# Performance work log

Measured on AMD Instinct MI355X. Metric: run time of the kernel, lower is better.

The kernel has to match this reference:

```python
import math
import jax, jax.numpy as jnp
import numpy as np

NUM_HEADS = 16


def setup_inputs() -> dict:
    key = jax.random.key(0)
    ks = jax.random.split(key, 5)
    B, S, H = 2, 2048, 1024
    hidden_states = jax.random.normal(ks[0], (B, S, H), dtype=jnp.float32)
    # causal lower-triangular float mask [1, 1, S, S], as the module expects
    ltor_mask = jnp.tril(jnp.ones((S, S), dtype=jnp.float32))[None, None, :, :]
    # weights stored pre-transposed: y = x @ W + b (equivalent to torch Linear)
    W_qkv = jax.random.normal(ks[1], (H, 3 * H), dtype=jnp.float32) * (1.0 / math.sqrt(H))
    b_qkv = jnp.zeros((3 * H,), dtype=jnp.float32)
    W_dense = jax.random.normal(ks[2], (H, H), dtype=jnp.float32) * (1.0 / math.sqrt(H))
    b_dense = jnp.zeros((H,), dtype=jnp.float32)
    return {
        "hidden_states": hidden_states,
        "ltor_mask": ltor_mask,
        "W_qkv": W_qkv,
        "b_qkv": b_qkv,
        "W_dense": W_dense,
        "b_dense": b_dense,
    }


def reference(hidden_states, ltor_mask, W_qkv, b_qkv, W_dense, b_dense):
    B, S, H = hidden_states.shape
    nh = NUM_HEADS
    hd = H // nh

    # fused QKV projection: [B, S, 3H] -> split -> [B, nh, S, hd]
    qkv = hidden_states @ W_qkv + b_qkv
    q, k, v = jnp.split(qkv, 3, axis=-1)

    def to_heads(x):
        return x.reshape(B, S, nh, hd).transpose(0, 2, 1, 3)

    q, k, v = to_heads(q), to_heads(k), to_heads(v)

    # scaled dot-product scores [B, nh, S, S]
    scores = jnp.einsum("bhqd,bhkd->bhqk", q, k) / math.sqrt(hd)
    # mul/sub causal masking, exactly as the torch module does
    scores = scores * ltor_mask - 10000.0 * (1.0 - ltor_mask)
    probs = jax.nn.softmax(scores, axis=-1)
    # attention dropout omitted (eval mode / p=0.0)

    ctx = jnp.einsum("bhqk,bhkd->bhqd", probs, v)
    ctx = ctx.transpose(0, 2, 1, 3).reshape(B, S, H)

    out = ctx @ W_dense + b_dense
    # output dropout omitted (eval mode / p=0.0)
    return out
```

## Files before the change

### kernel.cpp

```cpp
#include <hip/hip_runtime.h>
#include <math.h>

#define BATCH 2
#define SEQ   2048
#define HID   1024
#define NHEAD 16
#define HDIM  64
#define MTOT  (BATCH * SEQ)
#define QKVN  (3 * HID)
#define HBUF  ((size_t)BATCH * NHEAD * SEQ * HDIM)

typedef _Float16 f16x8 __attribute__((ext_vector_type(8)));
typedef _Float16 f16x4 __attribute__((ext_vector_type(4)));
typedef float    f32x4 __attribute__((ext_vector_type(4)));

#define MFMA16(a, b, c) __builtin_amdgcn_mfma_f32_16x16x32_f16((a), (b), (c), 0, 0, 0)

#define GLDS16(gp, lp) __builtin_amdgcn_global_load_lds( \
    (const __attribute__((address_space(1))) void*)(gp), \
    (__attribute__((address_space(3))) void*)(lp), 16, 0, 0)

#if __has_builtin(__builtin_amdgcn_exp2f)
#define EXP2F(x) __builtin_amdgcn_exp2f(x)
#else
#define EXP2F(x) exp2f(x)
#endif

#define SCALE2 0.18033688011f
#define MASK2  -14426.950408f
#define BIAS2  -4.0f

__global__ __launch_bounds__(256) void prep_kernel(
    const float* __restrict__ hs, const float* __restrict__ Wqkv,
    const float* __restrict__ Wd, _Float16* __restrict__ A_h,
    _Float16* __restrict__ outQ, _Float16* __restrict__ outD)
{
    __shared__ _Float16 T[32][36];
    const int gid = blockIdx.x;
    const int tid = threadIdx.x;
    if (gid < 2048) {
        const int ci = gid * 256 + tid;
        const int m = ci >> 7, cc = ci & 127;
        const int g = cc >> 2, c = cc & 3;
        const float* src = hs + (size_t)m * 1024 + cc * 8;
        f16x8 o;
#pragma unroll
        for (int j = 0; j < 8; ++j) o[j] = (_Float16)src[j];
        *(f16x8*)(A_h + (size_t)m * 1024 + g * 32 + ((c ^ (m & 3)) << 3)) = o;
        return;
    }
    const int tb = gid - 2048;
    const int bx = tb & 127, k0 = (tb >> 7) * 32;
    const float* in;
    _Float16* out;
    int N, n0;
    if (bx < 96) { in = Wqkv; out = outQ; N = QKVN; n0 = bx * 32; }
    else         { in = Wd;   out = outD; N = HID;  n0 = (bx - 96) * 32; }
    {
        const int r = tid >> 3, c4 = (tid & 7) * 4;
        float4 v = *(const float4*)(in + (size_t)(k0 + r) * N + n0 + c4);
        T[r][c4 + 0] = (_Float16)v.x;
        T[r][c4 + 1] = (_Float16)v.y;
        T[r][c4 + 2] = (_Float16)v.z;
        T[r][c4 + 3] = (_Float16)v.w;
    }
    __syncthreads();
    {
        const int nn = tid >> 3, k4 = (tid & 7) * 4;
        const int n = n0 + nn;
        f16x4 o;
        o[0] = T[k4 + 0][nn]; o[1] = T[k4 + 1][nn];
        o[2] = T[k4 + 2][nn]; o[3] = T[k4 + 3][nn];
        const int pos = ((k4 >> 3) ^ (n & 3)), half = (k4 >> 2) & 1;
        *(f16x4*)(out + (size_t)n * 1024 + k0 + pos * 8 + half * 4) = o;
    }
}

template<int EPI, int TM>
__global__ __launch_bounds__(256) void mfma_gemm(
    const _Float16* __restrict__ A, const _Float16* __restrict__ Bt,
    const float* __restrict__ bias, void* __restrict__ Cout,
    int M, int N, int K)
{
    __shared__ _Float16 As[TM * 32];
    __shared__ _Float16 Bs[128 * 32];
    constexpr int TI = TM / 32;
    constexpr int AR = TM / 4;

    const int tid = threadIdx.x;
    const int w = tid >> 6, l = tid & 63;
    const int a = l & 15, q4 = l >> 4;
    const int m0 = blockIdx.y * TM, n0 = blockIdx.x * 128;
    const int wm = (w >> 1) * (TM / 2), wn = (w & 1) * 64;

    f32x4 acc[TI][4];
#pragma unroll
    for (int i = 0; i < TI; ++i)
#pragma unroll
        for (int j = 0; j < 4; ++j) acc[i][j] = (f32x4){0.f, 0.f, 0.f, 0.f};

    const _Float16* gA = A + (size_t)(m0 + w * AR + (l >> 2)) * K + (l & 3) * 8;
    const _Float16* gB = Bt + (size_t)(n0 + w * 32 + (l >> 2)) * K + (l & 3) * 8;
    _Float16* sA = As + w * AR * 32;
    _Float16* sB = Bs + w * 1024;

    for (int k0 = 0; k0 < K; k0 += 32) {
#pragma unroll
        for (int u = 0; u < TM / 64; ++u)
            GLDS16(gA + (size_t)u * 16 * K + k0, sA + u * 512);
        GLDS16(gB + k0,          sB);
        GLDS16(gB + 16 * K + k0, sB + 512);
        __syncthreads();

        f16x8 af[TI], bf[4];
        const int pa = (q4 ^ (a & 3)) << 3;
#pragma unroll
        for (int i = 0; i < TI; ++i)
            af[i] = *(const f16x8*)&As[(wm + 16 * i + a) * 32 + pa];
#pragma unroll
        for (int j = 0; j < 4; ++j)
            bf[j] = *(const f16x8*)&Bs[(wn + 16 * j + a) * 32 + pa];
#pragma unroll
        for (int i = 0; i < TI; ++i)
#pragma unroll
            for (int j = 0; j < 4; ++j)
                acc[i][j] = MFMA16(af[i], bf[j], acc[i][j]);
        __syncthreads();
    }

    if (EPI == 0) {
        _Float16* base = (_Float16*)Cout;
#pragma unroll
        for (int j = 0; j < 4; ++j) {
            const int n = n0 + wn + 16 * j + a;
            const float bv = bias[n];
            const int t = n >> 10, h = (n >> 6) & 15, d = n & 63;
#pragma unroll
            for (int i = 0; i < TI; ++i) {
                const int mb = m0 + wm + 16 * i + q4 * 4;
                const int bb = mb >> 11, sb = mb & 2047;
                if (t == 2) {
                    f16x4 ov;
#pragma unroll
                    for (int r = 0; r < 4; ++r)
                        ov[r] = (_Float16)(acc[i][j][r] + bv);
                    const size_t off =
                        ((size_t)((bb * 16 + h) * 64 + d)) * 2048
                        + (sb & ~63)
                        + ((((sb >> 3) & 7) ^ (d & 7)) << 3) + (sb & 7);
                    *(f16x4*)(base + 3 * HBUF + off) = ov;
                } else if (t == 1) {
#pragma unroll
                    for (int r = 0; r < 4; ++r) {
                        const int s = sb + r;
                        const _Float16 val = (_Float16)(acc[i][j][r] + bv);
                        const int dk = ((((d >> 3) ^ (s & 7)) & 7) << 3) | (d & 7);
                        base[HBUF + ((size_t)(bb * 16 + h) * 2048 + s) * 64 + dk] = val;
                    }
                } else {
#pragma unroll
                    for (int r = 0; r < 4; ++r) {
                        const _Float16 val = (_Float16)(acc[i][j][r] + bv);
                        base[((size_t)(bb * 16 + h) * 2048 + sb + r) * 64 + d] = val;
                    }
                }
            }
        }
    } else {
        float* C = (float*)Cout;
#pragma unroll
        for (int j = 0; j < 4; ++j) {
            const int n = n0 + wn + 16 * j + a;
            const float bv = bias[n];
#pragma unroll
            for (int i = 0; i < TI; ++i)
#pragma unroll
                for (int r = 0; r < 4; ++r) {
                    const int m = m0 + wm + 16 * i + q4 * 4 + r;
                    C[(size_t)m * N + n] = acc[i][j][r] + bv;
                }
        }
    }
}

__global__ __launch_bounds__(256, 2) void attn_mfma(
    const _Float16* __restrict__ qb, const _Float16* __restrict__ kb,
    const _Float16* __restrict__ vtb, _Float16* __restrict__ ctx)
{
    __shared__ _Float16 Ks[2][64 * 64];
    __shared__ _Float16 VT[2][64 * 64];
    __shared__ _Float16 Ps[4][16 * 64];

    const int bid = blockIdx.x;
    const int jj = bid >> 3;
    const int bhIdx = (bid & 7) * 4 + (jj >> 4);
    const int p = jj & 15;
    const int b = bhIdx >> 4, h = bhIdx & 15;
    const int tid = threadIdx.x;
    const int w = tid >> 6, l = tid & 63;
    const int a = l & 15, q4 = l >> 4, a7 = a & 7;
    const size_t bh  = ((size_t)b * NHEAD + h) * SEQ;
    const size_t bhd = ((size_t)b * NHEAD + h) * 64;

    const int qHi = (31 - p) * 64 + w * 16;
    const int qLo = p * 64 + w * 16;
    const int ntiles = 32 - p;

    f16x8 qfh[2], qfl[2];
    {
        const _Float16* qp = qb + (bh + qHi + a) * 64;
        qfh[0] = *(const f16x8*)(qp + q4 * 8);
        qfh[1] = *(const f16x8*)(qp + 32 + q4 * 8);
        const _Float16* ql = qb + (bh + qLo + a) * 64;
        qfl[0] = *(const f16x8*)(ql + q4 * 8);
        qfl[1] = *(const f16x8*)(ql + 32 + q4 * 8);
    }

    f32x4 Oh[4], Ol[4];
#pragma unroll
    for (int c = 0; c < 4; ++c) {
        Oh[c] = (f32x4){0.f, 0.f, 0.f, 0.f};
        Ol[c] = (f32x4){0.f, 0.f, 0.f, 0.f};
    }
    float lh = 0.f, ll = 0.f;

    const _Float16* kg = kb + (bh + w * 16) * 64 + l * 8;
    const int vrow = w * 16 + (l >> 3);
    const _Float16* vg = vtb + (bhd + vrow) * 2048 + (l & 7) * 8;
    _Float16* pbuf = &Ps[w][0];
    const int p0 = (q4 ^ a7) << 3;

    auto stage = [&](int t, int buf) {
        _Float16* ksl = &Ks[buf][0] + w * 1024 + l * 8;
        const _Float16* kt = kg + (size_t)t * 4096;
        GLDS16(kt,       ksl);
        GLDS16(kt + 512, ksl + 512);
        _Float16* vtl = &VT[buf][0] + vrow * 64 + (l & 7) * 8;
        GLDS16(vg + t * 64,            vtl);
        GLDS16(vg + t * 64 + 8 * 2048, vtl + 512);
    };

    stage(0, 0);

    for (int t = 0; t < ntiles; ++t) {
        __syncthreads();
        if (t + 1 < ntiles) stage(t + 1, (t + 1) & 1);

        const _Float16* ksb  = &Ks[t & 1][0];
        const _Float16* vbuf = &VT[t & 1][0];
        const int kt0 = t * 64;
        const bool doLo = (t <= p);

        f32x4 sh[4], sl[4];
#pragma unroll
        for (int n0 = 0; n0 < 4; ++n0) {
            f16x8 kf0 = *(const f16x8*)&ksb[(n0 * 16 + a) * 64 + p0];
            f16x8 kf1 = *(const f16x8*)&ksb[(n0 * 16 + a) * 64 + (p0 ^ 32)];
            f32x4 c = (f32x4){0.f, 0.f, 0.f, 0.f};
            c = MFMA16(kf0, qfh[0], c);
            c = MFMA16(kf1, qfh[1], c);
            sh[n0] = c;
            if (doLo) {
                f32x4 d = (f32x4){0.f, 0.f, 0.f, 0.f};
                d = MFMA16(kf0, qfl[0], d);
                d = MFMA16(kf1, qfl[1], d);
                sl[n0] = d;
            }
        }

        auto half_step = [&](f32x4 st[4], float& lrun, f32x4* O,
                             const bool maskT, const int qbase) {
            if (maskT) {
#pragma unroll
                for (int n0 = 0; n0 < 4; ++n0)
#pragma unroll
                    for (int r = 0; r < 4; ++r) {
                        const int kgl = kt0 + n0 * 16 + q4 * 4 + r;
                        st[n0][r] = (kgl > qbase + a) ? MASK2
                                                      : fmaf(st[n0][r], SCALE2, BIAS2);
                    }
            } else {
#pragma unroll
                for (int n0 = 0; n0 < 4; ++n0)
#pragma unroll
                    for (int r = 0; r < 4; ++r)
                        st[n0][r] = fmaf(st[n0][r], SCALE2, BIAS2);
            }
            float ls = 0.f;
#pragma unroll
            for (int n0 = 0; n0 < 4; ++n0)
#pragma unroll
                for (int r = 0; r < 4; ++r) {
                    const float pe = EXP2F(st[n0][r]);
                    st[n0][r] = pe;
                    ls += pe;
                }
            lrun += ls;
#pragma unroll
            for (int n0 = 0; n0 < 4; ++n0) {
                f16x4 pk;
#pragma unroll
                for (int r = 0; r < 4; ++r) pk[r] = (_Float16)st[n0][r];
                const int pos = (2 * n0 + (q4 >> 1)) ^ a7;
                *(f16x4*)&pbuf[a * 64 + pos * 8 + ((q4 & 1) << 2)] = pk;
            }
            f16x8 pf0 = *(const f16x8*)&pbuf[a * 64 + p0];
            f16x8 pf1 = *(const f16x8*)&pbuf[a * 64 + (p0 ^ 32)];
#pragma unroll
            for (int c = 0; c < 4; ++c) {
                f16x8 vf0 = *(const f16x8*)&vbuf[(c * 16 + a) * 64 + p0];
                f16x8 vf1 = *(const f16x8*)&vbuf[(c * 16 + a) * 64 + (p0 ^ 32)];
                O[c] = MFMA16(vf0, pf0, O[c]);
                O[c] = MFMA16(vf1, pf1, O[c]);
            }
        };

        half_step(sh, lh, Oh, t == 31 - p, qHi);
        if (doLo) half_step(sl, ll, Ol, t == p, qLo);
    }

    auto finish = [&](float lrun, const f32x4* O, const int qbase) {
        float lt = lrun;
        lt += __shfl_xor(lt, 16);
        lt += __shfl_xor(lt, 32);
        const float inv = 1.0f / lt;
        const size_t row = (size_t)b * SEQ + qbase + a;
#pragma unroll
        for (int c = 0; c < 4; ++c) {
            const int d0 = c * 16 + q4 * 4;
            const int kcol = h * 64 + (d0 & ~31)
                           + ((((d0 >> 3) & 3) ^ (a & 3)) << 3) + (d0 & 7);
            f16x4 ov;
#pragma unroll
            for (int r = 0; r < 4; ++r) ov[r] = (_Float16)(O[c][r] * inv);
            *(f16x4*)(ctx + row * HID + kcol) = ov;
        }
    };
    finish(lh, Oh, qHi);
    finish(ll, Ol, qLo);
}

extern "C" void kernel_launch(void* const* d_in, const int* in_sizes, int n_in,
                              void* d_out, int out_size, void* d_ws, size_t ws_size,
                              hipStream_t stream) {
    const float* hs   = (const float*)d_in[0];
    const float* Wqkv = (const float*)d_in[2];
    const float* bqkv = (const float*)d_in[3];
    const float* Wd   = (const float*)d_in[4];
    const float* bd   = (const float*)d_in[5];

    _Float16* A_h   = (_Float16*)d_ws;
    _Float16* WqkvT = A_h + (size_t)MTOT * HID;
    _Float16* WdT   = WqkvT + (size_t)QKVN * HID;
    _Float16* qbuf  = WdT + (size_t)HID * HID;
    _Float16* ctxb  = qbuf + 4 * HBUF;

    prep_kernel<<<6144, 256, 0, stream>>>(hs, Wqkv, Wd, A_h, WqkvT, WdT);

    mfma_gemm<0, 128><<<dim3(QKVN / 128, MTOT / 128), 256, 0, stream>>>(
        A_h, WqkvT, bqkv, (void*)qbuf, MTOT, QKVN, HID);

    attn_mfma<<<512, 256, 0, stream>>>(
        qbuf, qbuf + HBUF, qbuf + 3 * HBUF, ctxb);

    mfma_gemm<1, 64><<<dim3(HID / 128, MTOT / 64), 256, 0, stream>>>(
        ctxb, WdT, bd, d_out, MTOT, HID, HID);
}
```

Before: 194.4 us.

## Replace QKV GEMM with 256x256-tile 8-wave pipelined kernel using K=64 stages

Result: no change. 190.6 us (-2.0%).

```diff
diff --git a/kernel.cpp b/kernel.cpp
--- a/kernel.cpp
+++ b/kernel.cpp
@@ -41,12 +41,12 @@
     if (gid < 2048) {
         const int ci = gid * 256 + tid;
         const int m = ci >> 7, cc = ci & 127;
-        const int g = cc >> 2, c = cc & 3;
         const float* src = hs + (size_t)m * 1024 + cc * 8;
         f16x8 o;
 #pragma unroll
         for (int j = 0; j < 8; ++j) o[j] = (_Float16)src[j];
-        *(f16x8*)(A_h + (size_t)m * 1024 + g * 32 + ((c ^ (m & 3)) << 3)) = o;
+        *(f16x8*)(A_h + (size_t)m * 1024 + ((cc >> 3) << 6)
+                  + (((cc & 7) ^ (m & 7)) << 3)) = o;
         return;
     }
     const int tb = gid - 2048;
@@ -54,8 +54,9 @@
     const float* in;
     _Float16* out;
     int N, n0;
-    if (bx < 96) { in = Wqkv; out = outQ; N = QKVN; n0 = bx * 32; }
-    else         { in = Wd;   out = outD; N = HID;  n0 = (bx - 96) * 32; }
+    bool isQ;
+    if (bx < 96) { in = Wqkv; out = outQ; N = QKVN; n0 = bx * 32; isQ = true; }
+    else         { in = Wd;   out = outD; N = HID;  n0 = (bx - 96) * 32; isQ = false; }
     {
         const int r = tid >> 3, c4 = (tid & 7) * 4;
         float4 v = *(const float4*)(in + (size_t)(k0 + r) * N + n0 + c4);
@@ -71,8 +72,180 @@
         f16x4 o;
         o[0] = T[k4 + 0][nn]; o[1] = T[k4 + 1][nn];
         o[2] = T[k4 + 2][nn]; o[3] = T[k4 + 3][nn];
-        const int pos = ((k4 >> 3) ^ (n & 3)), half = (k4 >> 2) & 1;
-        *(f16x4*)(out + (size_t)n * 1024 + k0 + pos * 8 + half * 4) = o;
+        if (isQ) {
+            const int cin = (((k0 >> 5) & 1) << 2) | (k4 >> 3);
+            const int pos = cin ^ (n & 7);
+            *(f16x4*)(out + (size_t)n * 1024 + (k0 & ~63) + pos * 8 + (k4 & 7)) = o;
+        } else {
+            const int pos = ((k4 >> 3) ^ (n & 3)), half = (k4 >> 2) & 1;
+            *(f16x4*)(out + (size_t)n * 1024 + k0 + pos * 8 + half * 4) = o;
+        }
+    }
+}
+
+__global__ __launch_bounds__(512, 2) void qkv_gemm8(
+    const _Float16* __restrict__ A, const _Float16* __restrict__ Bt,
+    const float* __restrict__ bias, _Float16* __restrict__ base)
+{
+    __shared__ _Float16 S[2][2][16384];
+    const int tid = threadIdx.x;
+    const int w = tid >> 6, l = tid & 63;
+    const int a = l & 15, q4 = l >> 4, a7 = a & 7;
+    const int xc = blockIdx.x & 7, loc = blockIdx.x >> 3;
+    const int bx = (xc & 1) * 6 + loc % 6;
+    const int by = (xc >> 1) * 4 + loc / 6;
+    const int m0 = by * 256, n0 = bx * 256;
+    const int wm = (w >> 2) * 128, wn = (w & 3) * 64;
+
+    const int srow = tid >> 3;
+    const int scol = (tid & 7) * 8;
+    const _Float16* gAs = A  + (size_t)(m0 + srow) * 1024 + scol;
+    const _Float16* gBs = Bt + (size_t)(n0 + srow) * 1024 + scol;
+
+    auto stage_u = [&](int u, int kt, int sl) {
+        const size_t ko = (size_t)kt * 64;
+        if (u < 4)
+            GLDS16(gAs + (size_t)u * 65536 + ko, &S[sl][0][0] + u * 4096 + tid * 8);
+        else
+            GLDS16(gBs + (size_t)(u - 4) * 65536 + ko, &S[sl][1][0] + (u - 4) * 4096 + tid * 8);
+    };
+
+#pragma unroll
+    for (int u = 0; u < 8; ++u) stage_u(u, 0, 0);
+#pragma unroll
+    for (int u = 0; u < 8; ++u) stage_u(u, 1, 1);
+    asm volatile("s_waitcnt vmcnt(8)" ::: "memory");
+    __builtin_amdgcn_sched_barrier(0);
+    __builtin_amdgcn_s_barrier();
+
+    f32x4 acc[8][4];
+#pragma unroll
+    for (int i = 0; i < 8; ++i)
+#pragma unroll
+        for (int j = 0; j < 4; ++j) acc[i][j] = (f32x4){0.f, 0.f, 0.f, 0.f};
+
+#define FRG(SP, row_, ks_) \
+    (*(const f16x8*)&(SP)[(row_) * 64 + ((((ks_) * 4 + q4) ^ a7) << 3)])
+
+    for (int t = 0; t < 16; ++t) {
+        const int sl = t & 1, nsl = sl ^ 1;
+        const _Float16* sA = &S[sl][0][0];
+        const _Float16* sB = &S[sl][1][0];
+        const bool st = (t >= 1) & (t < 15);
+
+        f16x8 afL[4][2], afH[4][2], bfL[2][2], bfH[2][2];
+
+#pragma unroll
+        for (int i = 0; i < 4; ++i) {
+            afL[i][0] = FRG(sA, wm + i * 16 + a, 0);
+            afL[i][1] = FRG(sA, wm + i * 16 + a, 1);
+        }
+#pragma unroll
+        for (int j = 0; j < 2; ++j) {
+            bfL[j][0] = FRG(sB, wn + j * 16 + a, 0);
+            bfL[j][1] = FRG(sB, wn + j * 16 + a, 1);
+        }
+        if (st) { stage_u(0, t + 1, nsl); stage_u(1, t + 1, nsl); stage_u(2, t + 1, nsl); }
+        __builtin_amdgcn_s_barrier();
+        asm volatile("s_waitcnt lgkmcnt(0)" ::: "memory");
+        __builtin_amdgcn_s_setprio(1);
+#pragma unroll
+        for (int i = 0; i < 4; ++i)
+#pragma unroll
+            for (int j = 0; j < 2; ++j) {
+                acc[i][j] = MFMA16(afL[i][0], bfL[j][0], acc[i][j]);
+                acc[i][j] = MFMA16(afL[i][1], bfL[j][1], acc[i][j]);
+            }
+        __builtin_amdgcn_s_setprio(0);
+        __builtin_amdgcn_s_barrier();
+
+#pragma unroll
+        for (int j = 0; j < 2; ++j) {
+            bfH[j][0] = FRG(sB, wn + 32 + j * 16 + a, 0);
+            bfH[j][1] = FRG(sB, wn + 32 + j * 16 + a, 1);
+        }
+        if (st) { stage_u(3, t + 1, nsl); stage_u(4, t + 1, nsl); stage_u(5, t + 1, nsl); }
+        __builtin_amdgcn_s_barrier();
+        asm volatile("s_waitcnt lgkmcnt(0)" ::: "memory");
+        __builtin_amdgcn_s_setprio(1);
+#pragma unroll
+        for (int i = 0; i < 4; ++i)
+#pragma unroll
+            for (int j = 0; j < 2; ++j) {
+                acc[i][j + 2] = MFMA16(afL[i][0], bfH[j][0], acc[i][j + 2]);
+                acc[i][j + 2] = MFMA16(afL[i][1], bfH[j][1], acc[i][j + 2]);
+            }
+        __builtin_amdgcn_s_setprio(0);
+        __builtin_amdgcn_s_barrier();
+
+#pragma unroll
+        for (int i = 0; i < 4; ++i) {
+            afH[i][0] = FRG(sA, wm + 64 + i * 16 + a, 0);
+            afH[i][1] = FRG(sA, wm + 64 + i * 16 + a, 1);
+        }
+        if (st) { stage_u(6, t + 1, nsl); stage_u(7, t + 1, nsl); }
+        __builtin_amdgcn_s_barrier();
+        asm volatile("s_waitcnt lgkmcnt(0)" ::: "memory");
+        __builtin_amdgcn_s_setprio(1);
+#pragma unroll
+        for (int i = 0; i < 4; ++i)
+#pragma unroll
+            for (int j = 0; j < 2; ++j) {
+                acc[i + 4][j + 2] = MFMA16(afH[i][0], bfH[j][0], acc[i + 4][j + 2]);
+                acc[i + 4][j + 2] = MFMA16(afH[i][1], bfH[j][1], acc[i + 4][j + 2]);
+            }
+        __builtin_amdgcn_s_setprio(0);
+        __builtin_amdgcn_s_barrier();
+
+        __builtin_amdgcn_s_setprio(1);
+#pragma unroll
+        for (int i = 0; i < 4; ++i)
+#pragma unroll
+            for (int j = 0; j < 2; ++j) {
+                acc[i + 4][j] = MFMA16(afH[i][0], bfL[j][0], acc[i + 4][j]);
+                acc[i + 4][j] = MFMA16(afH[i][1], bfL[j][1], acc[i + 4][j]);
+            }
+        __builtin_amdgcn_s_setprio(0);
+        asm volatile("s_waitcnt vmcnt(0)" ::: "memory");
+        __builtin_amdgcn_sched_barrier(0);
+        __builtin_amdgcn_s_barrier();
+    }
+#undef FRG
+
+#pragma unroll
+    for (int j = 0; j < 4; ++j) {
+        const int n = n0 + wn + 16 * j + a;
+        const float bv = bias[n];
+        const int tq = n >> 10, h = (n >> 6) & 15, d = n & 63;
+#pragma unroll
+        for (int i = 0; i < 8; ++i) {
+            const int mb = m0 + wm + 16 * i + q4 * 4;
+            const int bb = mb >> 11, sb = mb & 2047;
+            if (tq == 2) {
+                f16x4 ov;
+#pragma unroll
+                for (int r = 0; r < 4; ++r) ov[r] = (_Float16)(acc[i][j][r] + bv);
+                const size_t off =
+                    ((size_t)((bb * 16 + h) * 64 + d)) * 2048
+                    + (sb & ~63)
+                    + ((((sb >> 3) & 7) ^ (d & 7)) << 3) + (sb & 7);
+                *(f16x4*)(base + 3 * HBUF + off) = ov;
+            } else if (tq == 1) {
+#pragma unroll
+                for (int r = 0; r < 4; ++r) {
+                    const int s = sb + r;
+                    const _Float16 val = (_Float16)(acc[i][j][r] + bv);
+                    const int dk = ((((d >> 3) ^ (s & 7)) & 7) << 3) | (d & 7);
+                    base[HBUF + ((size_t)(bb * 16 + h) * 2048 + s) * 64 + dk] = val;
+                }
+            } else {
+#pragma unroll
+                for (int r = 0; r < 4; ++r) {
+                    const _Float16 val = (_Float16)(acc[i][j][r] + bv);
+                    base[((size_t)(bb * 16 + h) * 2048 + sb + r) * 64 + d] = val;
+                }
+            }
+        }
     }
 }
 
@@ -128,45 +301,7 @@
         __syncthreads();
     }
 
-    if (EPI == 0) {
-        _Float16* base = (_Float16*)Cout;
-#pragma unroll
-        for (int j = 0; j < 4; ++j) {
-            const int n = n0 + wn + 16 * j + a;
-            const float bv = bias[n];
-            const int t = n >> 10, h = (n >> 6) & 15, d = n & 63;
-#pragma unroll
-            for (int i = 0; i < TI; ++i) {
-                const int mb = m0 + wm + 16 * i + q4 * 4;
-                const int bb = mb >> 11, sb = mb & 2047;
-                if (t == 2) {
-                    f16x4 ov;
-#pragma unroll
-                    for (int r = 0; r < 4; ++r)
-                        ov[r] = (_Float16)(acc[i][j][r] + bv);
-                    const size_t off =
-                        ((size_t)((bb * 16 + h) * 64 + d)) * 2048
-                        + (sb & ~63)
-                        + ((((sb >> 3) & 7) ^ (d & 7)) << 3) + (sb & 7);
-                    *(f16x4*)(base + 3 * HBUF + off) = ov;
-                } else if (t == 1) {
-#pragma unroll
-                    for (int r = 0; r < 4; ++r) {
-                        const int s = sb + r;
-                        const _Float16 val = (_Float16)(acc[i][j][r] + bv);
-                        const int dk = ((((d >> 3) ^ (s & 7)) & 7) << 3) | (d & 7);
-                        base[HBUF + ((size_t)(bb * 16 + h) * 2048 + s) * 64 + dk] = val;
-                    }
-                } else {
-#pragma unroll
-                    for (int r = 0; r < 4; ++r) {
-                        const _Float16 val = (_Float16)(acc[i][j][r] + bv);
-                        base[((size_t)(bb * 16 + h) * 2048 + sb + r) * 64 + d] = val;
-                    }
-                }
-            }
-        }
-    } else {
+    {
         float* C = (float*)Cout;
 #pragma unroll
         for (int j = 0; j < 4; ++j) {
@@ -357,8 +492,7 @@
 
     prep_kernel<<<6144, 256, 0, stream>>>(hs, Wqkv, Wd, A_h, WqkvT, WdT);
 
-    mfma_gemm<0, 128><<<dim3(QKVN / 128, MTOT / 128), 256, 0, stream>>>(
-        A_h, WqkvT, bqkv, (void*)qbuf, MTOT, QKVN, HID);
+    qkv_gemm8<<<192, 512, 0, stream>>>(A_h, WqkvT, bqkv, qbuf);
 
     attn_mfma<<<512, 256, 0, stream>>>(
         qbuf, qbuf + HBUF, qbuf + 3 * HBUF, ctxb);
```

## Replace QKV GEMM with 256x256-tile, 4-stage pipelined 512-thread MFMA kernel

Applied to the files above, without the earlier changes.

After: 189.1 us. -2.7%, faster.

```diff
diff --git a/kernel.cpp b/kernel.cpp
--- a/kernel.cpp
+++ b/kernel.cpp
@@ -41,12 +41,11 @@
     if (gid < 2048) {
         const int ci = gid * 256 + tid;
         const int m = ci >> 7, cc = ci & 127;
-        const int g = cc >> 2, c = cc & 3;
         const float* src = hs + (size_t)m * 1024 + cc * 8;
         f16x8 o;
 #pragma unroll
         for (int j = 0; j < 8; ++j) o[j] = (_Float16)src[j];
-        *(f16x8*)(A_h + (size_t)m * 1024 + g * 32 + ((c ^ (m & 3)) << 3)) = o;
+        *(f16x8*)(A_h + (size_t)m * 1024 + cc * 8) = o;
         return;
     }
     const int tb = gid - 2048;
@@ -54,8 +53,9 @@
     const float* in;
     _Float16* out;
     int N, n0;
-    if (bx < 96) { in = Wqkv; out = outQ; N = QKVN; n0 = bx * 32; }
-    else         { in = Wd;   out = outD; N = HID;  n0 = (bx - 96) * 32; }
+    bool isQ;
+    if (bx < 96) { in = Wqkv; out = outQ; N = QKVN; n0 = bx * 32; isQ = true; }
+    else         { in = Wd;   out = outD; N = HID;  n0 = (bx - 96) * 32; isQ = false; }
     {
         const int r = tid >> 3, c4 = (tid & 7) * 4;
         float4 v = *(const float4*)(in + (size_t)(k0 + r) * N + n0 + c4);
@@ -71,8 +71,157 @@
         f16x4 o;
         o[0] = T[k4 + 0][nn]; o[1] = T[k4 + 1][nn];
         o[2] = T[k4 + 2][nn]; o[3] = T[k4 + 3][nn];
-        const int pos = ((k4 >> 3) ^ (n & 3)), half = (k4 >> 2) & 1;
-        *(f16x4*)(out + (size_t)n * 1024 + k0 + pos * 8 + half * 4) = o;
+        if (isQ) {
+            *(f16x4*)(out + (size_t)n * 1024 + k0 + k4) = o;
+        } else {
+            const int pos = ((k4 >> 3) ^ (n & 3)), half = (k4 >> 2) & 1;
+            *(f16x4*)(out + (size_t)n * 1024 + k0 + pos * 8 + half * 4) = o;
+        }
+    }
+}
+
+__global__ __launch_bounds__(512, 2) void qkv_gemm8(
+    const _Float16* __restrict__ A, const _Float16* __restrict__ Bt,
+    const float* __restrict__ bias, _Float16* __restrict__ base)
+{
+    __shared__ _Float16 S[4][2][8192];
+    const int tid = threadIdx.x;
+    const int w = tid >> 6, l = tid & 63;
+    const int a = l & 15, q4 = l >> 4;
+    const int xc = blockIdx.x & 7, loc = blockIdx.x >> 3;
+    const int bx = (xc & 1) * 6 + loc % 6;
+    const int by = (xc >> 1) * 4 + loc / 6;
+    const int m0 = by * 256, n0 = bx * 256;
+    const int wm = (w >> 2) * 128, wn = (w & 3) * 64;
+
+    const int csw = (((tid & 3) ^ ((tid >> 3) & 3)) << 3);
+    const _Float16* gAs = A  + (size_t)(m0 + (tid >> 2)) * 1024 + csw;
+    const _Float16* gBs = Bt + (size_t)(n0 + (tid >> 2)) * 1024 + csw;
+
+    auto stage_tile = [&](int kt) {
+        const int s = kt & 3;
+        const size_t ko = (size_t)kt * 32;
+        GLDS16(gAs + ko,          &S[s][0][0] + tid * 8);
+        GLDS16(gAs + 131072 + ko, &S[s][0][0] + 4096 + tid * 8);
+        GLDS16(gBs + ko,          &S[s][1][0] + tid * 8);
+        GLDS16(gBs + 131072 + ko, &S[s][1][0] + 4096 + tid * 8);
+    };
+
+    stage_tile(0); stage_tile(1); stage_tile(2);
+    asm volatile("s_waitcnt vmcnt(8)" ::: "memory");
+    __builtin_amdgcn_sched_barrier(0);
+    __builtin_amdgcn_s_barrier();
+    __builtin_amdgcn_sched_barrier(0);
+
+    f32x4 acc[8][4];
+#pragma unroll
+    for (int i = 0; i < 8; ++i)
+#pragma unroll
+        for (int j = 0; j < 4; ++j) acc[i][j] = (f32x4){0.f, 0.f, 0.f, 0.f};
+
+    const int pc = ((q4 ^ ((a >> 1) & 3)) << 3);
+#define FRG(SP, row_) (*(const f16x8*)&(SP)[(row_) * 32 + pc])
+
+    f16x8 af[8], bf[4];
+    {
+        const _Float16* sA = &S[0][0][0];
+        const _Float16* sB = &S[0][1][0];
+#pragma unroll
+        for (int i = 0; i < 4; ++i) af[i] = FRG(sA, wm + i * 16 + a);
+        bf[0] = FRG(sB, wn + a);
+        bf[1] = FRG(sB, wn + 16 + a);
+    }
+
+#pragma unroll 4
+    for (int t = 0; t < 32; ++t) {
+        const _Float16* sA = &S[t & 3][0][0];
+        const _Float16* sB = &S[t & 3][1][0];
+        if (t <= 28) stage_tile(t + 3);
+
+        __builtin_amdgcn_s_setprio(1);
+#pragma unroll
+        for (int i = 0; i < 4; ++i)
+#pragma unroll
+            for (int j = 0; j < 2; ++j)
+                acc[i][j] = MFMA16(af[i], bf[j], acc[i][j]);
+        __builtin_amdgcn_s_setprio(0);
+
+        bf[2] = FRG(sB, wn + 32 + a);
+        bf[3] = FRG(sB, wn + 48 + a);
+        __builtin_amdgcn_s_setprio(1);
+#pragma unroll
+        for (int i = 0; i < 4; ++i)
+#pragma unroll
+            for (int j = 0; j < 2; ++j)
+                acc[i][j + 2] = MFMA16(af[i], bf[j + 2], acc[i][j + 2]);
+        __builtin_amdgcn_s_setprio(0);
+
+#pragma unroll
+        for (int i = 0; i < 4; ++i) af[i + 4] = FRG(sA, wm + 64 + i * 16 + a);
+        __builtin_amdgcn_s_setprio(1);
+#pragma unroll
+        for (int i = 0; i < 4; ++i)
+#pragma unroll
+            for (int j = 0; j < 2; ++j)
+                acc[i + 4][j + 2] = MFMA16(af[i + 4], bf[j + 2], acc[i + 4][j + 2]);
+#pragma unroll
+        for (int i = 0; i < 4; ++i)
+#pragma unroll
+            for (int j = 0; j < 2; ++j)
+                acc[i + 4][j] = MFMA16(af[i + 4], bf[j], acc[i + 4][j]);
+        __builtin_amdgcn_s_setprio(0);
+
+        if (t < 31) {
+            if (t <= 28)      asm volatile("s_waitcnt vmcnt(8)" ::: "memory");
+            else if (t == 29) asm volatile("s_waitcnt vmcnt(4)" ::: "memory");
+            else              asm volatile("s_waitcnt vmcnt(0)" ::: "memory");
+            __builtin_amdgcn_sched_barrier(0);
+            __builtin_amdgcn_s_barrier();
+            __builtin_amdgcn_sched_barrier(0);
+            const _Float16* nA = &S[(t + 1) & 3][0][0];
+            const _Float16* nB = &S[(t + 1) & 3][1][0];
+#pragma unroll
+            for (int i = 0; i < 4; ++i) af[i] = FRG(nA, wm + i * 16 + a);
+            bf[0] = FRG(nB, wn + a);
+            bf[1] = FRG(nB, wn + 16 + a);
+        }
+    }
+#undef FRG
+
+#pragma unroll
+    for (int j = 0; j < 4; ++j) {
+        const int n = n0 + wn + 16 * j + a;
+        const float bv = bias[n];
+        const int tq = n >> 10, h = (n >> 6) & 15, d = n & 63;
+#pragma unroll
+        for (int i = 0; i < 8; ++i) {
+            const int mb = m0 + wm + 16 * i + q4 * 4;
+            const int bb = mb >> 11, sb = mb & 2047;
+            if (tq == 2) {
+                f16x4 ov;
+#pragma unroll
+                for (int r = 0; r < 4; ++r) ov[r] = (_Float16)(acc[i][j][r] + bv);
+                const size_t off =
+                    ((size_t)((bb * 16 + h) * 64 + d)) * 2048
+                    + (sb & ~63)
+                    + ((((sb >> 3) & 7) ^ (d & 7)) << 3) + (sb & 7);
+                *(f16x4*)(base + 3 * HBUF + off) = ov;
+            } else if (tq == 1) {
+#pragma unroll
+                for (int r = 0; r < 4; ++r) {
+                    const int s = sb + r;
+                    const _Float16 val = (_Float16)(acc[i][j][r] + bv);
+                    const int dk = ((((d >> 3) ^ (s & 7)) & 7) << 3) | (d & 7);
+                    base[HBUF + ((size_t)(bb * 16 + h) * 2048 + s) * 64 + dk] = val;
+                }
+            } else {
+#pragma unroll
+                for (int r = 0; r < 4; ++r) {
+                    const _Float16 val = (_Float16)(acc[i][j][r] + bv);
+                    base[((size_t)(bb * 16 + h) * 2048 + sb + r) * 64 + d] = val;
+                }
+            }
+        }
     }
 }
 
@@ -128,45 +277,7 @@
         __syncthreads();
     }
 
-    if (EPI == 0) {
-        _Float16* base = (_Float16*)Cout;
-#pragma unroll
-        for (int j = 0; j < 4; ++j) {
-            const int n = n0 + wn + 16 * j + a;
-            const float bv = bias[n];
-            const int t = n >> 10, h = (n >> 6) & 15, d = n & 63;
-#pragma unroll
-            for (int i = 0; i < TI; ++i) {
-                const int mb = m0 + wm + 16 * i + q4 * 4;
-                const int bb = mb >> 11, sb = mb & 2047;
-                if (t == 2) {
-                    f16x4 ov;
-#pragma unroll
-                    for (int r = 0; r < 4; ++r)
-                        ov[r] = (_Float16)(acc[i][j][r] + bv);
-                    const size_t off =
-                        ((size_t)((bb * 16 + h) * 64 + d)) * 2048
-                        + (sb & ~63)
-                        + ((((sb >> 3) & 7) ^ (d & 7)) << 3) + (sb & 7);
-                    *(f16x4*)(base + 3 * HBUF + off) = ov;
-                } else if (t == 1) {
-#pragma unroll
-                    for (int r = 0; r < 4; ++r) {
-                        const int s = sb + r;
-                        const _Float16 val = (_Float16)(acc[i][j][r] + bv);
-                        const int dk = ((((d >> 3) ^ (s & 7)) & 7) << 3) | (d & 7);
-                        base[HBUF + ((size_t)(bb * 16 + h) * 2048 + s) * 64 + dk] = val;
-                    }
-                } else {
-#pragma unroll
-                    for (int r = 0; r < 4; ++r) {
-                        const _Float16 val = (_Float16)(acc[i][j][r] + bv);
-                        base[((size_t)(bb * 16 + h) * 2048 + sb + r) * 64 + d] = val;
-                    }
-                }
-            }
-        }
-    } else {
+    {
         float* C = (float*)Cout;
 #pragma unroll
         for (int j = 0; j < 4; ++j) {
@@ -357,8 +468,7 @@
 
     prep_kernel<<<6144, 256, 0, stream>>>(hs, Wqkv, Wd, A_h, WqkvT, WdT);
 
-    mfma_gemm<0, 128><<<dim3(QKVN / 128, MTOT / 128), 256, 0, stream>>>(
-        A_h, WqkvT, bqkv, (void*)qbuf, MTOT, QKVN, HID);
+    qkv_gemm8<<<192, 512, 0, stream>>>(A_h, WqkvT, bqkv, qbuf);
 
     attn_mfma<<<512, 256, 0, stream>>>(
         qbuf, qbuf + HBUF, qbuf + 3 * HBUF, ctxb);
```
